# Kernel optimization log

Measured on AMD Instinct MI355X. Metric: run time of the kernel, lower is better.

Reference implementation:

```python
import jax, jax.numpy as jnp
import numpy as np

B, P, C, O = 64, 8732, 81, 16
THRESH = 0.5
NEGPOS = 3
VAR0, VAR1 = 0.1, 0.2


def setup_inputs() -> dict:
    key = jax.random.key(0)
    k1, k2, k3, k4, k5, k6, k7 = jax.random.split(key, 7)
    # ground-truth boxes in point form (xmin,ymin,xmax,ymax), valid and inside [0,1]
    lo = jax.random.uniform(k1, (B, O, 2), minval=0.0, maxval=0.7)
    wh = jax.random.uniform(k2, (B, O, 2), minval=0.05, maxval=0.3)
    truths = jnp.concatenate([lo, lo + wh], axis=-1)
    labels = jax.random.randint(k3, (B, O), 0, C - 1).astype(jnp.int32)
    # prior boxes in center-size form with strictly positive w/h
    ctr = jax.random.uniform(k4, (P, 2), minval=0.05, maxval=0.95)
    pwh = jax.random.uniform(k5, (P, 2), minval=0.05, maxval=0.5)
    dbox = jnp.concatenate([ctr, pwh], axis=-1)
    loc_data = jax.random.normal(k6, (B, P, 4), dtype=jnp.float32)
    conf_data = jax.random.normal(k7, (B, P, C), dtype=jnp.float32)
    return {"loc_data": loc_data, "conf_data": conf_data, "dbox": dbox,
            "truths": truths, "labels": labels}


def point_form(boxes):
    return jnp.concatenate([boxes[:, :2] - boxes[:, 2:] / 2,
                            boxes[:, :2] + boxes[:, 2:] / 2], axis=1)


def jaccard(box_a, box_b):
    # box_a: [A,4], box_b: [B,4] point form -> IoU [A,B]
    max_xy = jnp.minimum(box_a[:, None, 2:], box_b[None, :, 2:])
    min_xy = jnp.maximum(box_a[:, None, :2], box_b[None, :, :2])
    inter = jnp.prod(jnp.clip(max_xy - min_xy, 0.0, None), axis=-1)  # [A,B]
    area_a = jnp.prod(box_a[:, 2:] - box_a[:, :2], axis=-1)[:, None]
    area_b = jnp.prod(box_b[:, 2:] - box_b[:, :2], axis=-1)[None, :]
    return inter / (area_a + area_b - inter)


def encode(matched, priors):
    g_cxcy = ((matched[:, :2] + matched[:, 2:]) / 2 - priors[:, :2]) / (VAR0 * priors[:, 2:])
    g_wh = jnp.log((matched[:, 2:] - matched[:, :2]) / priors[:, 2:]) / VAR1
    return jnp.concatenate([g_cxcy, g_wh], axis=1)


def match_one(truths, labels, priors, priors_pf):
    overlaps = jaccard(truths, priors_pf)                  # [O, P]
    best_prior_idx = jnp.argmax(overlaps, axis=1)          # [O]
    best_truth_overlap = jnp.max(overlaps, axis=0)         # [P]
    best_truth_idx = jnp.argmax(overlaps, axis=0)          # [P]
    best_truth_overlap = best_truth_overlap.at[best_prior_idx].set(2.0)
    best_truth_idx = best_truth_idx.at[best_prior_idx].set(jnp.arange(truths.shape[0]))
    matches = truths[best_truth_idx]                       # [P,4]
    conf = jnp.where(best_truth_overlap < THRESH, 0, labels[best_truth_idx] + 1)
    loc = encode(matches, priors)                          # [P,4]
    return loc, conf


def reference(loc_data, conf_data, dbox, truths, labels):
    priors_pf = point_form(dbox)
    loc_t, conf_t = jax.vmap(match_one, in_axes=(0, 0, None, None))(
        truths, labels, dbox, priors_pf)                   # [B,P,4], [B,P]

    pos_mask = conf_t > 0                                  # [B,P]
    # localization smooth-L1 (beta=1) over positive priors
    d = jnp.abs(loc_data - loc_t)
    sl1 = jnp.where(d < 1.0, 0.5 * d * d, d - 0.5)
    loss_l = jnp.sum(sl1 * pos_mask[..., None].astype(sl1.dtype))

    # per-prior cross entropy
    logz = jax.nn.logsumexp(conf_data, axis=-1)            # [B,P]
    picked = jnp.take_along_axis(conf_data, conf_t[..., None], axis=-1)[..., 0]
    ce = logz - picked                                     # [B,P]

    # hard negative mining: rank negatives by CE (positives zeroed)
    loss_c_neg = jnp.where(pos_mask, 0.0, ce)
    order = jnp.argsort(-loss_c_neg, axis=1)
    idx_rank = jnp.argsort(order, axis=1)
    num_pos = jnp.sum(pos_mask, axis=1, keepdims=True)     # [B,1]
    num_neg = jnp.clip(num_pos * NEGPOS, None, P)
    neg_mask = idx_rank < num_neg

    sel = (pos_mask | neg_mask).astype(ce.dtype)
    loss_c = jnp.sum(ce * sel)

    N = jnp.sum(num_pos).astype(loss_l.dtype)
    return loss_l / N, loss_c / N
```

## Files before the change

kernel.cpp:

```cpp
#include <hip/hip_runtime.h>
#include <stdint.h>
#include <math.h>

#define B 64
#define P 8732
#define C 81
#define O 16
#define THRESH 0.5f
#define NEGPOS 3
#define VAR0 0.1f
#define VAR1 0.2f

#define ITER 4
#define ROWS_PER_WAVE (8 * ITER)
#define ROWS_PER_BLOCK (4 * ROWS_PER_WAVE)

__global__ __launch_bounds__(256) void bp_k(const float* __restrict__ dbox,
                                            const float* __restrict__ truths,
                                            int* __restrict__ forced_p,
                                            int* __restrict__ num_pos,
                                            float* __restrict__ possum,
                                            float* __restrict__ lossl,
                                            float* __restrict__ acc,
                                            int* __restrict__ done) {
    const int tid = threadIdx.x;
    if (blockIdx.x == 0) {
        if (tid < B) { num_pos[tid] = 0; possum[tid] = 0.f; lossl[tid] = 0.f; }
        if (tid == B) { acc[0] = 0.f; acc[1] = 0.f; }
        if (tid == B + 1) { *done = 0; }
    }
    const int lane = tid & 63;
    const int gw = blockIdx.x * 4 + (tid >> 6);
    const int b = gw >> 4, o = gw & 15;
    const float4 t = *(const float4*)(truths + (size_t)(b * O + o) * 4);
    const float ta = (t.z - t.x) * (t.w - t.y);

    unsigned long long best = 0ull;
    for (int p0 = lane; p0 < P; p0 += 256) {
#pragma unroll
        for (int u = 0; u < 4; ++u) {
            const int p = p0 + 64 * u;
            if (p < P) {
                const float4 db = *(const float4*)(dbox + (size_t)p * 4);
                const float px0 = db.x - db.z * 0.5f, py0 = db.y - db.w * 0.5f;
                const float px1 = db.x + db.z * 0.5f, py1 = db.y + db.w * 0.5f;
                const float parea = (px1 - px0) * (py1 - py0);
                float ix = fminf(t.z, px1) - fmaxf(t.x, px0);
                float iy = fminf(t.w, py1) - fmaxf(t.y, py0);
                ix = fmaxf(ix, 0.f); iy = fmaxf(iy, 0.f);
                const float inter = ix * iy;
                const float ov = inter / (ta + parea - inter);
                const unsigned long long key =
                    ((unsigned long long)__float_as_uint(ov) << 32) |
                    (unsigned long long)(0xFFFFFFFFu - (unsigned)p);
                if (key > best) best = key;
            }
        }
    }
    for (int off = 32; off; off >>= 1) {
        const unsigned long long o2 = __shfl_xor(best, off);
        if (o2 > best) best = o2;
    }
    if (lane == 0)
        forced_p[b * O + o] = (int)(0xFFFFFFFFu - (unsigned)(best & 0xFFFFFFFFull));
}

__global__ __launch_bounds__(256) void loss_k(
        const float* __restrict__ loc_data,
        const float* __restrict__ conf_data,
        const float* __restrict__ dbox,
        const float* __restrict__ truths,
        const int* __restrict__ labels,
        const int* __restrict__ forced_p,
        float* __restrict__ negce,
        int* __restrict__ num_pos, float* __restrict__ possum,
        float* __restrict__ lossl) {
    const int b = blockIdx.y;
    const int tid = threadIdx.x;
    const int lane = tid & 63;
    const int wid = tid >> 6;
    const int sub = lane & 15;
    const int gbase = lane & 48;

    __shared__ float s_truth[O * 4];
    __shared__ float s_l, s_p;
    __shared__ int s_n;
    if (tid < O * 4) s_truth[tid] = truths[b * O * 4 + tid];
    if (tid == 0) { s_l = 0.f; s_p = 0.f; s_n = 0; }

    const float4 tt = *(const float4*)(truths + (size_t)(b * O + sub) * 4);
    const int f_reg = forced_p[b * O + sub];
    const int lab_reg = labels[b * O + sub];
    const float tarea = (tt.z - tt.x) * (tt.w - tt.y);
    __syncthreads();

    float l_acc = 0.f;
    float p_acc = 0.f;
    int n_acc = 0;

    const int wbase = blockIdx.x * ROWS_PER_BLOCK + wid * ROWS_PER_WAVE;

    for (int r = 0; r < ITER; ++r) {
        const int pA = wbase + 8 * r + (gbase >> 4);
        const int pB = pA + 4;
        const bool actA = (pA < P), actB = (pB < P);
        const int dA = actA ? pA : P - 1;
        const int dB = actB ? pB : P - 1;
        const size_t rowA = (size_t)b * P + dA;
        const size_t rowB = (size_t)b * P + dB;

        const float* rpA = conf_data + rowA * C;
        const float* rpB = conf_data + rowB * C;
        const float4 qA = *(const float4*)(rpA + 4 * sub);
        const float4 qB = *(const float4*)(rpB + 4 * sub);
        const float eA = rpA[64 + sub];
        const float eB = rpB[64 + sub];
        const float e80A = rpA[80];
        const float e80B = rpB[80];
        const float4 dbA = *(const float4*)(dbox + (size_t)dA * 4);
        const float4 dbB = *(const float4*)(dbox + (size_t)dB * 4);

        float ovA, ovB;
        int tiA = sub, tiB = sub;
        {
            const float pax0 = dbA.x - dbA.z * 0.5f, pay0 = dbA.y - dbA.w * 0.5f;
            const float pax1 = dbA.x + dbA.z * 0.5f, pay1 = dbA.y + dbA.w * 0.5f;
            const float pareaA = (pax1 - pax0) * (pay1 - pay0);
            float ixA = fminf(tt.z, pax1) - fmaxf(tt.x, pax0);
            float iyA = fminf(tt.w, pay1) - fmaxf(tt.y, pay0);
            ixA = fmaxf(ixA, 0.f); iyA = fmaxf(iyA, 0.f);
            const float interA = ixA * iyA;
            ovA = interA / (tarea + pareaA - interA);

            const float pbx0 = dbB.x - dbB.z * 0.5f, pby0 = dbB.y - dbB.w * 0.5f;
            const float pbx1 = dbB.x + dbB.z * 0.5f, pby1 = dbB.y + dbB.w * 0.5f;
            const float pareaB = (pbx1 - pbx0) * (pby1 - pby0);
            float ixB = fminf(tt.z, pbx1) - fmaxf(tt.x, pbx0);
            float iyB = fminf(tt.w, pby1) - fmaxf(tt.y, pby0);
            ixB = fmaxf(ixB, 0.f); iyB = fmaxf(iyB, 0.f);
            const float interB = ixB * iyB;
            ovB = interB / (tarea + pareaB - interB);
        }
        for (int off = 8; off; off >>= 1) {
            const float oA = __shfl_xor(ovA, off);
            const int iA = __shfl_xor(tiA, off);
            const float oB = __shfl_xor(ovB, off);
            const int iB = __shfl_xor(tiB, off);
            if (oA > ovA || (oA == ovA && iA < tiA)) { ovA = oA; tiA = iA; }
            if (oB > ovB || (oB == ovB && iB < tiB)) { ovB = oB; tiB = iB; }
        }
        const unsigned long long balA = __ballot(f_reg == pA);
        const unsigned long long balB = __ballot(f_reg == pB);
        const unsigned mA = (unsigned)(balA >> gbase) & 0xFFFFu;
        const unsigned mB = (unsigned)(balB >> gbase) & 0xFFFFu;
        const bool fA = (mA != 0), fB = (mB != 0);
        if (fA) tiA = 31 - __clz(mA);
        if (fB) tiB = 31 - __clz(mB);
        const int labA = __shfl(lab_reg, gbase | tiA);
        const int labB = __shfl(lab_reg, gbase | tiB);
        const int confA = (fA || ovA >= THRESH) ? (labA + 1) : 0;
        const int confB = (fB || ovB >= THRESH) ? (labB + 1) : 0;
        const bool posA = confA > 0, posB = confB > 0;

        float sA = __expf(qA.x) + __expf(qA.y) + __expf(qA.z) + __expf(qA.w) + __expf(eA);
        float sB = __expf(qB.x) + __expf(qB.y) + __expf(qB.z) + __expf(qB.w) + __expf(eB);
        for (int off = 8; off; off >>= 1) {
            sA += __shfl_xor(sA, off);
            sB += __shfl_xor(sB, off);
        }
        sA += __expf(e80A);
        sB += __expf(e80B);

        const float selA = (confA < 64)
            ? ((confA & 2) ? ((confA & 1) ? qA.w : qA.z) : ((confA & 1) ? qA.y : qA.x))
            : eA;
        const float selB = (confB < 64)
            ? ((confB & 2) ? ((confB & 1) ? qB.w : qB.z) : ((confB & 1) ? qB.y : qB.x))
            : eB;
        const int hA = (confA < 64) ? (confA >> 2) : (confA & 15);
        const int hB = (confB < 64) ? (confB >> 2) : (confB & 15);
        float pkA = __shfl(selA, gbase | hA);
        float pkB = __shfl(selB, gbase | hB);
        if (confA == 80) pkA = e80A;
        if (confB == 80) pkB = e80B;

        const float cevA = __logf(sA) - pkA;
        const float cevB = __logf(sB) - pkB;

        if (actA && sub == 0) {
            negce[rowA] = posA ? 0.f : cevA;
            if (posA) { p_acc += cevA; n_acc++; }
        }
        if (actB && sub == 0) {
            negce[rowB] = posB ? 0.f : cevB;
            if (posB) { p_acc += cevB; n_acc++; }
        }
        if (actA && posA && sub < 4) {
            const float mx0 = s_truth[tiA * 4 + 0], my0 = s_truth[tiA * 4 + 1];
            const float mx1 = s_truth[tiA * 4 + 2], my1 = s_truth[tiA * 4 + 3];
            float tgt;
            if (sub == 0)      tgt = ((mx0 + mx1) * 0.5f - dbA.x) / (VAR0 * dbA.z);
            else if (sub == 1) tgt = ((my0 + my1) * 0.5f - dbA.y) / (VAR0 * dbA.w);
            else if (sub == 2) tgt = logf((mx1 - mx0) / dbA.z) / VAR1;
            else               tgt = logf((my1 - my0) / dbA.w) / VAR1;
            const float d = fabsf(loc_data[rowA * 4 + sub] - tgt);
            l_acc += (d < 1.f) ? 0.5f * d * d : d - 0.5f;
        }
        if (actB && posB && sub < 4) {
            const float mx0 = s_truth[tiB * 4 + 0], my0 = s_truth[tiB * 4 + 1];
            const float mx1 = s_truth[tiB * 4 + 2], my1 = s_truth[tiB * 4 + 3];
            float tgt;
            if (sub == 0)      tgt = ((mx0 + mx1) * 0.5f - dbB.x) / (VAR0 * dbB.z);
            else if (sub == 1) tgt = ((my0 + my1) * 0.5f - dbB.y) / (VAR0 * dbB.w);
            else if (sub == 2) tgt = logf((mx1 - mx0) / dbB.z) / VAR1;
            else               tgt = logf((my1 - my0) / dbB.w) / VAR1;
            const float d = fabsf(loc_data[rowB * 4 + sub] - tgt);
            l_acc += (d < 1.f) ? 0.5f * d * d : d - 0.5f;
        }
    }
    for (int off = 32; off; off >>= 1) {
        l_acc += __shfl_xor(l_acc, off);
        p_acc += __shfl_xor(p_acc, off);
        n_acc += __shfl_xor(n_acc, off);
    }
    if (lane == 0) {
        atomicAdd(&s_l, l_acc);
        atomicAdd(&s_p, p_acc);
        atomicAdd(&s_n, n_acc);
    }
    __syncthreads();
    if (tid == 0) {
        atomicAdd(&lossl[b], s_l);
        atomicAdd(&possum[b], s_p);
        atomicAdd(&num_pos[b], s_n);
    }
}

__global__ __launch_bounds__(1024) void mine_k(
        const float* __restrict__ negce,
        const int* __restrict__ num_pos,
        const float* __restrict__ possum,
        const float* __restrict__ lossl,
        float* __restrict__ acc, int* __restrict__ done,
        float* __restrict__ out) {
    const int b = blockIdx.x;
    const int tid = threadIdx.x;
    const int lane = tid & 63;
    const int wid = tid >> 6;
    const float* x = negce + (size_t)b * P;
    float v[9];
#pragma unroll
    for (int j = 0; j < 9; ++j) {
        const int i = tid + j * 1024;
        v[j] = (i < P) ? x[i] : -1.0f;
    }
    int k = num_pos[b] * NEGPOS;
    if (k > P) k = P;

    __shared__ int wred[2][16];
    __shared__ float wsumf[16];
    __shared__ int wcnt[16];
    float S = 0.f;
    if (k > 0) {
        unsigned lo = 0u, hi = 0x7F800000u;
        int parity = 0;
        while (lo < hi) {
            const unsigned mid = lo + ((hi - lo) >> 1);
            const float t = __uint_as_float(mid);
            int cnt = 0;
#pragma unroll
            for (int j = 0; j < 9; ++j) cnt += (v[j] > t) ? 1 : 0;
            for (int off = 32; off; off >>= 1) cnt += __shfl_xor(cnt, off);
            if (lane == 0) wred[parity][wid] = cnt;
            __syncthreads();
            int total = 0;
#pragma unroll
            for (int w = 0; w < 16; ++w) total += wred[parity][w];
            if (total < k) hi = mid; else lo = mid + 1;
            parity ^= 1;
        }
        const float t = __uint_as_float(lo);
        float sum = 0.f;
        int cnt = 0;
#pragma unroll
        for (int j = 0; j < 9; ++j) {
            if (v[j] > t) { sum += v[j]; cnt++; }
        }
        for (int off = 32; off; off >>= 1) {
            sum += __shfl_xor(sum, off);
            cnt += __shfl_xor(cnt, off);
        }
        if (lane == 0) { wsumf[wid] = sum; wcnt[wid] = cnt; }
        __syncthreads();
        if (tid == 0) {
            float ts = 0.f; int tc = 0;
#pragma unroll
            for (int w = 0; w < 16; ++w) { ts += wsumf[w]; tc += wcnt[w]; }
            S = ts + (float)(k - tc) * t;
        }
    }
    if (tid == 0) {
        atomicAdd(&acc[1], possum[b] + S);
        __threadfence();
        const int prev = atomicAdd(done, 1);
        if (prev == B - 1) {
            __threadfence();
            float N = 0.f, L = 0.f;
            for (int i = 0; i < B; ++i) { N += (float)num_pos[i]; L += lossl[i]; }
            const float cval = atomicAdd(&acc[1], 0.0f);
            out[0] = L / N;
            out[1] = cval / N;
        }
    }
}

extern "C" void kernel_launch(void* const* d_in, const int* in_sizes, int n_in,
                              void* d_out, int out_size, void* d_ws, size_t ws_size,
                              hipStream_t stream) {
    (void)in_sizes; (void)n_in; (void)out_size; (void)ws_size;
    const float* loc_data  = (const float*)d_in[0];
    const float* conf_data = (const float*)d_in[1];
    const float* dbox      = (const float*)d_in[2];
    const float* truths    = (const float*)d_in[3];
    const int*   labels    = (const int*)d_in[4];
    float* out = (float*)d_out;

    int* forced_p = (int*)d_ws;
    float* negce  = (float*)(forced_p + B * O);
    int* num_pos  = (int*)(negce + (size_t)B * P);
    float* possum = (float*)(num_pos + B);
    float* lossl  = possum + B;
    float* acc    = lossl + B;
    int* done     = (int*)(acc + 2);

    bp_k<<<(B * O) / 4, 256, 0, stream>>>(dbox, truths, forced_p,
                                          num_pos, possum, lossl, acc, done);
    loss_k<<<dim3((P + ROWS_PER_BLOCK - 1) / ROWS_PER_BLOCK, B), 256, 0, stream>>>(
        loc_data, conf_data, dbox, truths, labels, forced_p,
        negce, num_pos, possum, lossl);
    mine_k<<<B, 1024, 0, stream>>>(negce, num_pos, possum, lossl, acc, done, out);
}
```

Before: 367.3 us.

## Fuse hard-negative mining into loss kernel via last-block-per-batch election

Removes the separate mine_k launch. Each loss block increments a per-batch counter, and the last block to finish for a batch runs the bisection top-k selection with 256 threads holding 35 values each. Negative-CE stores and loads become agent-scope atomics so the electing block sees every other block's writes. This saves one launch and its gap, but the mining now runs on a single 256-thread block per batch with more registers per thread, and the extra registers may lower occupancy for the loss phase.

```diff
diff --git a/kernel.cpp b/kernel.cpp
--- a/kernel.cpp
+++ b/kernel.cpp
@@ -14,6 +14,9 @@
 #define ITER 4
 #define ROWS_PER_WAVE (8 * ITER)
 #define ROWS_PER_BLOCK (4 * ROWS_PER_WAVE)
+#define NBLK ((P + ROWS_PER_BLOCK - 1) / ROWS_PER_BLOCK)
+
+#define MJ 35
 
 __global__ __launch_bounds__(256) void bp_k(const float* __restrict__ dbox,
                                             const float* __restrict__ truths,
@@ -22,10 +25,11 @@
                                             float* __restrict__ possum,
                                             float* __restrict__ lossl,
                                             float* __restrict__ acc,
-                                            int* __restrict__ done) {
+                                            int* __restrict__ done,
+                                            int* __restrict__ done_b) {
     const int tid = threadIdx.x;
     if (blockIdx.x == 0) {
-        if (tid < B) { num_pos[tid] = 0; possum[tid] = 0.f; lossl[tid] = 0.f; }
+        if (tid < B) { num_pos[tid] = 0; possum[tid] = 0.f; lossl[tid] = 0.f; done_b[tid] = 0; }
         if (tid == B) { acc[0] = 0.f; acc[1] = 0.f; }
         if (tid == B + 1) { *done = 0; }
     }
@@ -65,7 +69,7 @@
         forced_p[b * O + o] = (int)(0xFFFFFFFFu - (unsigned)(best & 0xFFFFFFFFull));
 }
 
-__global__ __launch_bounds__(256) void loss_k(
+__global__ __launch_bounds__(256) void loss_mine_k(
         const float* __restrict__ loc_data,
         const float* __restrict__ conf_data,
         const float* __restrict__ dbox,
@@ -74,7 +78,10 @@
         const int* __restrict__ forced_p,
         float* __restrict__ negce,
         int* __restrict__ num_pos, float* __restrict__ possum,
-        float* __restrict__ lossl) {
+        float* __restrict__ lossl,
+        float* __restrict__ acc, int* __restrict__ done,
+        int* __restrict__ done_b,
+        float* __restrict__ out) {
     const int b = blockIdx.y;
     const int tid = threadIdx.x;
     const int lane = tid & 63;
@@ -85,6 +92,7 @@
     __shared__ float s_truth[O * 4];
     __shared__ float s_l, s_p;
     __shared__ int s_n;
+    __shared__ int s_mine;
     if (tid < O * 4) s_truth[tid] = truths[b * O * 4 + tid];
     if (tid == 0) { s_l = 0.f; s_p = 0.f; s_n = 0; }
 
@@ -188,11 +196,13 @@
         const float cevB = __logf(sB) - pkB;
 
         if (actA && sub == 0) {
-            negce[rowA] = posA ? 0.f : cevA;
+            __hip_atomic_store(&negce[rowA], posA ? 0.f : cevA,
+                               __ATOMIC_RELAXED, __HIP_MEMORY_SCOPE_AGENT);
             if (posA) { p_acc += cevA; n_acc++; }
         }
         if (actB && sub == 0) {
-            negce[rowB] = posB ? 0.f : cevB;
+            __hip_atomic_store(&negce[rowB], posB ? 0.f : cevB,
+                               __ATOMIC_RELAXED, __HIP_MEMORY_SCOPE_AGENT);
             if (posB) { p_acc += cevB; n_acc++; }
         }
         if (actA && posA && sub < 4) {
@@ -233,83 +243,90 @@
         atomicAdd(&lossl[b], s_l);
         atomicAdd(&possum[b], s_p);
         atomicAdd(&num_pos[b], s_n);
-    }
-}
-
-__global__ __launch_bounds__(1024) void mine_k(
-        const float* __restrict__ negce,
-        const int* __restrict__ num_pos,
-        const float* __restrict__ possum,
-        const float* __restrict__ lossl,
-        float* __restrict__ acc, int* __restrict__ done,
-        float* __restrict__ out) {
-    const int b = blockIdx.x;
-    const int tid = threadIdx.x;
-    const int lane = tid & 63;
-    const int wid = tid >> 6;
-    const float* x = negce + (size_t)b * P;
-    float v[9];
-#pragma unroll
-    for (int j = 0; j < 9; ++j) {
-        const int i = tid + j * 1024;
-        v[j] = (i < P) ? x[i] : -1.0f;
-    }
-    int k = num_pos[b] * NEGPOS;
-    if (k > P) k = P;
-
-    __shared__ int wred[2][16];
-    __shared__ float wsumf[16];
-    __shared__ int wcnt[16];
-    float S = 0.f;
-    if (k > 0) {
-        unsigned lo = 0u, hi = 0x7F800000u;
-        int parity = 0;
-        while (lo < hi) {
-            const unsigned mid = lo + ((hi - lo) >> 1);
-            const float t = __uint_as_float(mid);
+        __threadfence();
+        const int prev = __hip_atomic_fetch_add(&done_b[b], 1,
+                             __ATOMIC_ACQ_REL, __HIP_MEMORY_SCOPE_AGENT);
+        s_mine = (prev == NBLK - 1) ? 1 : 0;
+    }
+    __syncthreads();
+
+    if (s_mine) {
+        if (tid == 0) __threadfence();
+        __syncthreads();
+        const float* xb = negce + (size_t)b * P;
+        float v[MJ];
+#pragma unroll
+        for (int j = 0; j < MJ; ++j) {
+            const int i = tid + j * 256;
+            v[j] = (i < P)
+                 ? __hip_atomic_load(&xb[i], __ATOMIC_RELAXED, __HIP_MEMORY_SCOPE_AGENT)
+                 : -1.0f;
+        }
+        int k = __hip_atomic_load(&num_pos[b], __ATOMIC_RELAXED,
+                                  __HIP_MEMORY_SCOPE_AGENT) * NEGPOS;
+        if (k > P) k = P;
+
+        __shared__ int wred[2][4];
+        __shared__ float wsumf[4];
+        __shared__ int wcnt[4];
+        float S = 0.f;
+        if (k > 0) {
+            unsigned lo = 0u, hi = 0x7F800000u;
+            int parity = 0;
+            while (lo < hi) {
+                const unsigned mid = lo + ((hi - lo) >> 1);
+                const float t = __uint_as_float(mid);
+                int cnt = 0;
+#pragma unroll
+                for (int j = 0; j < MJ; ++j) cnt += (v[j] > t) ? 1 : 0;
+                for (int off = 32; off; off >>= 1) cnt += __shfl_xor(cnt, off);
+                if (lane == 0) wred[parity][wid] = cnt;
+                __syncthreads();
+                int total = 0;
+#pragma unroll
+                for (int w = 0; w < 4; ++w) total += wred[parity][w];
+                if (total < k) hi = mid; else lo = mid + 1;
+                parity ^= 1;
+            }
+            const float t = __uint_as_float(lo);
+            float sum = 0.f;
             int cnt = 0;
 #pragma unroll
-            for (int j = 0; j < 9; ++j) cnt += (v[j] > t) ? 1 : 0;
-            for (int off = 32; off; off >>= 1) cnt += __shfl_xor(cnt, off);
-            if (lane == 0) wred[parity][wid] = cnt;
+            for (int j = 0; j < MJ; ++j) {
+                if (v[j] > t) { sum += v[j]; cnt++; }
+            }
+            for (int off = 32; off; off >>= 1) {
+                sum += __shfl_xor(sum, off);
+                cnt += __shfl_xor(cnt, off);
+            }
+            if (lane == 0) { wsumf[wid] = sum; wcnt[wid] = cnt; }
             __syncthreads();
-            int total = 0;
-#pragma unroll
-            for (int w = 0; w < 16; ++w) total += wred[parity][w];
-            if (total < k) hi = mid; else lo = mid + 1;
-            parity ^= 1;
-        }
-        const float t = __uint_as_float(lo);
-        float sum = 0.f;
-        int cnt = 0;
-#pragma unroll
-        for (int j = 0; j < 9; ++j) {
-            if (v[j] > t) { sum += v[j]; cnt++; }
-        }
-        for (int off = 32; off; off >>= 1) {
-            sum += __shfl_xor(sum, off);
-            cnt += __shfl_xor(cnt, off);
-        }
-        if (lane == 0) { wsumf[wid] = sum; wcnt[wid] = cnt; }
-        __syncthreads();
+            if (tid == 0) {
+                float ts = 0.f; int tc = 0;
+#pragma unroll
+                for (int w = 0; w < 4; ++w) { ts += wsumf[w]; tc += wcnt[w]; }
+                S = ts + (float)(k - tc) * t;
+            }
+        }
         if (tid == 0) {
-            float ts = 0.f; int tc = 0;
-#pragma unroll
-            for (int w = 0; w < 16; ++w) { ts += wsumf[w]; tc += wcnt[w]; }
-            S = ts + (float)(k - tc) * t;
-        }
-    }
-    if (tid == 0) {
-        atomicAdd(&acc[1], possum[b] + S);
-        __threadfence();
-        const int prev = atomicAdd(done, 1);
-        if (prev == B - 1) {
+            const float psum = __hip_atomic_load(&possum[b], __ATOMIC_RELAXED,
+                                                 __HIP_MEMORY_SCOPE_AGENT);
+            atomicAdd(&acc[1], psum + S);
             __threadfence();
-            float N = 0.f, L = 0.f;
-            for (int i = 0; i < B; ++i) { N += (float)num_pos[i]; L += lossl[i]; }
-            const float cval = atomicAdd(&acc[1], 0.0f);
-            out[0] = L / N;
-            out[1] = cval / N;
+            const int prev2 = atomicAdd(done, 1);
+            if (prev2 == B - 1) {
+                __threadfence();
+                float N = 0.f, L = 0.f;
+                for (int i = 0; i < B; ++i) {
+                    N += (float)__hip_atomic_load(&num_pos[i], __ATOMIC_RELAXED,
+                                                  __HIP_MEMORY_SCOPE_AGENT);
+                    L += __hip_atomic_load(&lossl[i], __ATOMIC_RELAXED,
+                                           __HIP_MEMORY_SCOPE_AGENT);
+                }
+                const float cval = atomicAdd(&acc[1], 0.0f);
+                out[0] = L / N;
+                out[1] = cval / N;
+            }
         }
     }
 }
@@ -332,11 +349,11 @@
     float* lossl  = possum + B;
     float* acc    = lossl + B;
     int* done     = (int*)(acc + 2);
+    int* done_b   = done + 1;
 
     bp_k<<<(B * O) / 4, 256, 0, stream>>>(dbox, truths, forced_p,
-                                          num_pos, possum, lossl, acc, done);
-    loss_k<<<dim3((P + ROWS_PER_BLOCK - 1) / ROWS_PER_BLOCK, B), 256, 0, stream>>>(
+                                          num_pos, possum, lossl, acc, done, done_b);
+    loss_mine_k<<<dim3(NBLK, B), 256, 0, stream>>>(
         loc_data, conf_data, dbox, truths, labels, forced_p,
-        negce, num_pos, possum, lossl);
-    mine_k<<<B, 1024, 0, stream>>>(negce, num_pos, possum, lossl, acc, done, out);
+        negce, num_pos, possum, lossl, acc, done, done_b, out);
 }
```

After: 716.4 us. 1.95x slower.
